# Optimization experiments

Hardware: AMD Instinct MI355X
Metric: run time of the kernel (lower is better)

Reference implementation:

```python
import jax, jax.numpy as jnp
import numpy as np

BN_EPS = 1e-5

def _bn(x, g, b, m, v):
    # eval-mode BatchNorm1d over channel dim of [B, C, N]
    scale = g / jnp.sqrt(v + BN_EPS)
    return (x - m[:, None]) * scale[:, None] + b[:, None]

def _conv1(W, x, b=None):
    # 1x1 Conv1d == channel matmul: W [O, C], x [B, C, N] -> [B, O, N]
    y = jnp.einsum('oc,bcn->bon', W, x)
    if b is not None:
        y = y + b[:, None]
    return y

def _sa_layer(x, wqk, wv, bv, wt, bt, g, b, m, v):
    # offset self-attention; q_conv and k_conv share weights
    xk = _conv1(wqk, x)                          # [B, D, N]
    xq = jnp.swapaxes(xk, 1, 2)                  # [B, N, D]
    xv = _conv1(wv, x, bv)                       # [B, D, N]
    energy = jnp.einsum('bnd,bdm->bnm', xq, xk)  # [B, N, N]
    attn = jax.nn.softmax(energy, axis=-1)
    attn = attn / (1e-9 + attn.sum(axis=1, keepdims=True))  # L1 renorm over dim=1
    x_r = jnp.einsum('bdn,bnm->bdm', xv, attn)   # [B, D, N]
    x_r = jax.nn.relu(_bn(_conv1(wt, x - x_r, bt), g, b, m, v))
    return x + x_r

def setup_inputs() -> dict:
    key = jax.random.key(0)
    ks = iter(jax.random.split(key, 64))
    B, Cin, N = 16, 3, 2048
    D, F, H1, OUT = 128, 1024, 512, 50
    def rn(shape, s=0.05):
        return jax.random.normal(next(ks), shape, dtype=jnp.float32) * s
    def var(shape):
        return jax.random.uniform(next(ks), shape, dtype=jnp.float32) * 0.5 + 0.5
    inp = {
        'x': jax.random.normal(next(ks), (B, Cin, N), dtype=jnp.float32),
        'w1': rn((D, Cin)), 'w2': rn((D, D)),
        'bn1_g': jnp.ones((D,)), 'bn1_b': jnp.zeros((D,)), 'bn1_m': rn((D,)), 'bn1_v': var((D,)),
        'bn2_g': jnp.ones((D,)), 'bn2_b': jnp.zeros((D,)), 'bn2_m': rn((D,)), 'bn2_v': var((D,)),
        'sa_wqk': rn((4, D, D)), 'sa_wv': rn((4, D, D)), 'sa_bv': rn((4, D)),
        'sa_wt': rn((4, D, D)), 'sa_bt': rn((4, D)),
        'sa_g': jnp.ones((4, D)), 'sa_b': jnp.zeros((4, D)), 'sa_m': rn((4, D)), 'sa_v': var((4, D)),
        'wf': rn((F, 4 * D)),
        'bnf_g': jnp.ones((F,)), 'bnf_b': jnp.zeros((F,)), 'bnf_m': rn((F,)), 'bnf_v': var((F,)),
        'ws1': rn((H1, 3 * F)), 'bs1': rn((H1,)),
        'bns1_g': jnp.ones((H1,)), 'bns1_b': jnp.zeros((H1,)), 'bns1_m': rn((H1,)), 'bns1_v': var((H1,)),
        'ws2': rn((OUT, H1)), 'bs2': rn((OUT,)),
        'bns2_g': jnp.ones((OUT,)), 'bns2_b': jnp.zeros((OUT,)), 'bns2_m': rn((OUT,)), 'bns2_v': var((OUT,)),
    }
    return inp

def reference(x, w1, w2, bn1_g, bn1_b, bn1_m, bn1_v, bn2_g, bn2_b, bn2_m, bn2_v,
              sa_wqk, sa_wv, sa_bv, sa_wt, sa_bt, sa_g, sa_b, sa_m, sa_v,
              wf, bnf_g, bnf_b, bnf_m, bnf_v,
              ws1, bs1, bns1_g, bns1_b, bns1_m, bns1_v,
              ws2, bs2, bns2_g, bns2_b, bns2_m, bns2_v):
    B, _, N = x.shape
    h = jax.nn.relu(_bn(_conv1(w1, x), bn1_g, bn1_b, bn1_m, bn1_v))
    h = jax.nn.relu(_bn(_conv1(w2, h), bn2_g, bn2_b, bn2_m, bn2_v))
    feats = []
    for i in range(4):
        h = _sa_layer(h, sa_wqk[i], sa_wv[i], sa_bv[i], sa_wt[i], sa_bt[i],
                      sa_g[i], sa_b[i], sa_m[i], sa_v[i])
        feats.append(h)
    cat = jnp.concatenate(feats, axis=1)                 # [B, 512, N]
    fused = _bn(_conv1(wf, cat), bnf_g, bnf_b, bnf_m, bnf_v)
    fused = jnp.where(fused >= 0, fused, 0.2 * fused)    # LeakyReLU(0.2)
    x_max = fused.max(axis=2)                            # [B, 1024]
    x_avg = fused.mean(axis=2)                           # [B, 1024]
    gmax = jnp.broadcast_to(x_max[:, :, None], (B, x_max.shape[1], N))
    gavg = jnp.broadcast_to(x_avg[:, :, None], (B, x_avg.shape[1], N))
    h = jnp.concatenate([fused, gmax, gavg], axis=1)     # [B, 3072, N]
    h = jax.nn.relu(_bn(_conv1(ws1, h, bs1), bns1_g, bns1_b, bns1_m, bns1_v))
    # dropout is identity in eval mode
    h = jax.nn.relu(_bn(_conv1(ws2, h, bs2), bns2_g, bns2_b, bns2_m, bns2_v))
    return h  # [B, out_channel, N]
```

## Files before the change

### kernel.cpp

```cpp
#include <hip/hip_runtime.h>
#include <cstdint>
#include <cstddef>

#define B_   16
#define N_   2048
#define D_   128
#define F_   1024
#define H1_  512
#define OUT_ 50

static constexpr float BN_EPS = 1e-5f;

typedef __attribute__((ext_vector_type(8))) short short8;
typedef __attribute__((ext_vector_type(4))) float f32x4;

__device__ inline unsigned short f2bf(float f) {
  union { float f; unsigned u; } v; v.f = f;
  unsigned r = v.u + 0x7fff + ((v.u >> 16) & 1);
  return (unsigned short)(r >> 16);
}
__device__ inline float bf2f(unsigned short h) {
  union { unsigned u; float f; } v; v.u = ((unsigned)h) << 16; return v.f;
}

__device__ inline void dma16(const unsigned short* g, unsigned short* l) {
  __builtin_amdgcn_global_load_lds(
      (const __attribute__((address_space(1))) unsigned int*)g,
      (__attribute__((address_space(3))) unsigned int*)l, 16, 0, 0);
}

__global__ void foldw_k(const float* __restrict__ W, int ldW,
                        const float* __restrict__ bias,
                        const float* __restrict__ g, const float* __restrict__ bb,
                        const float* __restrict__ m, const float* __restrict__ v,
                        unsigned short* __restrict__ Wb, float* __restrict__ biasF,
                        int O, int Opad, int K) {
  long i = (long)blockIdx.x * 256 + threadIdx.x;
  if (i >= (long)Opad * K) return;
  int o = (int)(i / K), k = (int)(i % K);
  float sc = 1.f, sh = 0.f;
  if (o < O && g) { sc = g[o] * rsqrtf(v[o] + BN_EPS); sh = bb[o] - m[o] * sc; }
  float w = (o < O) ? W[(long)o * ldW + k] * sc : 0.f;
  Wb[i] = f2bf(w);
  if (k == 0 && biasF) {
    float bf = 0.f;
    if (o < O) bf = (bias ? bias[o] : 0.f) * sc + sh;
    biasF[o] = bf;
  }
}

__global__ void conv1_k(const float* __restrict__ x, const float* __restrict__ w1,
                        const float* __restrict__ g, const float* __restrict__ bb,
                        const float* __restrict__ m, const float* __restrict__ v,
                        unsigned short* __restrict__ h0b) {
  int o = threadIdx.x, n = blockIdx.x, b = blockIdx.y;
  const float* xb = x + (long)b * 3 * N_;
  float val = w1[o * 3 + 0] * xb[n] + w1[o * 3 + 1] * xb[N_ + n] + w1[o * 3 + 2] * xb[2 * N_ + n];
  float sc = g[o] * rsqrtf(v[o] + BN_EPS);
  val = val * sc + (bb[o] - m[o] * sc);
  h0b[((long)b * N_ + n) * D_ + o] = f2bf(fmaxf(val, 0.f));
}

template <int TM>
__global__ __launch_bounds__(256, 4)
void gemm_tok(const unsigned short* __restrict__ Wb, int ldW,
              const unsigned short* __restrict__ A, long sA, int ldA,
              const float* __restrict__ biasF,
              const float* __restrict__ perBO, int ldPBO,
              const unsigned short* __restrict__ resH, long sRes, int ldRes,
              unsigned short* __restrict__ outH, long sOutH, int ldOutH,
              float* __restrict__ pmax, float* __restrict__ psum,
              int K, int act, int flags) {
  constexpr int MT = TM / 32;
  __shared__ unsigned short lAB[TM * 64 + 128 * 64];
  __shared__ float lpm[4][64], lps[4][64];
  unsigned short* lA = lAB;
  unsigned short* lB = lAB + TM * 64;
  unsigned short* lS = lAB;
  int tid = threadIdx.x;
  int n0 = blockIdx.x * TM, o0 = blockIdx.y * 128, b = blockIdx.z;
  int wave = tid >> 6, lane = tid & 63;
  int wr = wave >> 1, wc = wave & 1;
  int quad = lane >> 4, l15 = lane & 15;
  int rowL = lane >> 3;
  int kseg = (lane & 7) ^ rowL;
  const unsigned short* Ab = A + (long)b * sA + (long)n0 * ldA;
  const unsigned short* Wp = Wb + (long)o0 * ldW;

  f32x4 acc[MT][4];
  #pragma unroll
  for (int i = 0; i < MT; ++i)
    #pragma unroll
    for (int j = 0; j < 4; ++j) acc[i][j] = (f32x4){0.f, 0.f, 0.f, 0.f};

  for (int kc = 0; kc < K; kc += 64) {
    #pragma unroll
    for (int t = 0; t < 4; ++t) {
      int chunk = t * 4 + wave;
      dma16(Wp + (long)(chunk * 8 + rowL) * ldW + kc + kseg * 8, &lB[chunk * 512]);
      if (chunk < TM / 8)
        dma16(Ab + (long)(chunk * 8 + rowL) * ldA + kc + kseg * 8, &lA[chunk * 512]);
    }
    __syncthreads();
    #pragma unroll
    for (int kk = 0; kk < 2; ++kk) {
      short8 af[MT], bf[4];
      #pragma unroll
      for (int mt = 0; mt < MT; ++mt) {
        int r = wr * (TM / 2) + mt * 16 + l15;
        af[mt] = *(const short8*)&lA[r * 64 + (((kk * 4 + quad) ^ (l15 & 7)) * 8)];
      }
      #pragma unroll
      for (int ot = 0; ot < 4; ++ot) {
        int r = wc * 64 + ot * 16 + l15;
        bf[ot] = *(const short8*)&lB[r * 64 + (((kk * 4 + quad) ^ (l15 & 7)) * 8)];
      }
      #pragma unroll
      for (int mt = 0; mt < MT; ++mt)
        #pragma unroll
        for (int ot = 0; ot < 4; ++ot)
          acc[mt][ot] = __builtin_amdgcn_mfma_f32_16x16x32_bf16(bf[ot], af[mt], acc[mt][ot], 0, 0, 0);
    }
    __syncthreads();
  }

  bool doPool = (flags & 32) != 0;
  #pragma unroll
  for (int ot = 0; ot < 4; ++ot) {
    int obL = wc * 64 + ot * 16 + quad * 4;
    int ob = o0 + obL;
    float bi[4] = {0.f, 0.f, 0.f, 0.f};
    if (biasF) { float4 t = *(const float4*)&biasF[ob]; bi[0] = t.x; bi[1] = t.y; bi[2] = t.z; bi[3] = t.w; }
    if (perBO) {
      float4 t = *(const float4*)&perBO[(long)b * ldPBO + ob];
      bi[0] += t.x; bi[1] += t.y; bi[2] += t.z; bi[3] += t.w;
    }
    float pm4[4], ps4[4];
    #pragma unroll
    for (int r = 0; r < 4; ++r) { pm4[r] = -1e30f; ps4[r] = 0.f; }
    int g = obL >> 3, go = obL & 7;
    #pragma unroll
    for (int mt = 0; mt < MT; ++mt) {
      int nL = wr * (TM / 2) + mt * 16 + l15;
      float vals[4];
      #pragma unroll
      for (int r = 0; r < 4; ++r) {
        float val = acc[mt][ot][r] + bi[r];
        if (act == 1)      val = fmaxf(val, 0.f);
        else if (act == 2) val = (val >= 0.f) ? val : 0.2f * val;
        vals[r] = val;
      }
      if (flags & 16) {
        uint2 rv = *(const uint2*)&resH[(long)b * sRes + (long)(n0 + nL) * ldRes + ob];
        unsigned short rr[4];
        *(uint2*)rr = rv;
        #pragma unroll
        for (int r = 0; r < 4; ++r) vals[r] += bf2f(rr[r]);
      }
      unsigned short t4[4];
      #pragma unroll
      for (int r = 0; r < 4; ++r) {
        t4[r] = f2bf(vals[r]);
        if (doPool) { pm4[r] = fmaxf(pm4[r], vals[r]); ps4[r] += vals[r]; }
      }
      int gp = (g & 8) | ((g ^ (nL & 7)) & 7);
      *(uint2*)&lS[nL * 128 + gp * 8 + go] = *(uint2*)&t4[0];
    }
    if (doPool) {
      #pragma unroll
      for (int r = 0; r < 4; ++r) {
        float m = pm4[r], s = ps4[r];
        m = fmaxf(m, __shfl_xor(m, 1)); s += __shfl_xor(s, 1);
        m = fmaxf(m, __shfl_xor(m, 2)); s += __shfl_xor(s, 2);
        m = fmaxf(m, __shfl_xor(m, 4)); s += __shfl_xor(s, 4);
        m = fmaxf(m, __shfl_xor(m, 8)); s += __shfl_xor(s, 8);
        if (l15 == 0) { lpm[wave][ot * 16 + quad * 4 + r] = m; lps[wave][ot * 16 + quad * 4 + r] = s; }
      }
    }
  }
  __syncthreads();
  {
    int r0 = tid >> 4, s = tid & 15;
    #pragma unroll
    for (int it = 0; it < TM / 16; ++it) {
      int row = it * 16 + r0;
      int sp = (s & 8) | ((s ^ (row & 7)) & 7);
      short8 v = *(const short8*)&lS[row * 128 + sp * 8];
      *(short8*)&outH[(long)b * sOutH + (long)(n0 + row) * ldOutH + o0 + s * 8] = v;
    }
  }
  if (doPool && tid < 128) {
    int wcx = tid >> 6, ol = tid & 63;
    float m = fmaxf(lpm[wcx][ol], lpm[wcx + 2][ol]);
    float s = lps[wcx][ol] + lps[wcx + 2][ol];
    int o = o0 + wcx * 64 + ol;
    pmax[((long)b * 16 + blockIdx.x) * 1024 + o] = m;
    psum[((long)b * 16 + blockIdx.x) * 1024 + o] = s;
  }
}

template <int TM>
__global__ __launch_bounds__(256, 4)
void gemm_chan(const unsigned short* __restrict__ Wb, int ldW,
               const unsigned short* __restrict__ A, long sA, int ldA,
               const float* __restrict__ biasF,
               float* __restrict__ outF, long sOutF, int ldOutF,
               unsigned short* __restrict__ outH, long sOutH, int ldOutH,
               int K, int O, int act) {
  constexpr int MT = TM / 32;
  __shared__ unsigned short lA[TM * 64];
  __shared__ unsigned short lB[128 * 64];
  int tid = threadIdx.x;
  int n0 = blockIdx.x * TM, o0 = blockIdx.y * 128, b = blockIdx.z;
  int wave = tid >> 6, lane = tid & 63;
  int wr = wave >> 1, wc = wave & 1;
  int quad = lane >> 4, l15 = lane & 15;
  int rowL = lane >> 3;
  int kseg = (lane & 7) ^ rowL;
  const unsigned short* Ab = A + (long)b * sA + (long)n0 * ldA;
  const unsigned short* Wp = Wb + (long)o0 * ldW;

  f32x4 acc[MT][4];
  #pragma unroll
  for (int i = 0; i < MT; ++i)
    #pragma unroll
    for (int j = 0; j < 4; ++j) acc[i][j] = (f32x4){0.f, 0.f, 0.f, 0.f};

  for (int kc = 0; kc < K; kc += 64) {
    #pragma unroll
    for (int t = 0; t < 4; ++t) {
      int chunk = t * 4 + wave;
      dma16(Wp + (long)(chunk * 8 + rowL) * ldW + kc + kseg * 8, &lB[chunk * 512]);
      if (chunk < TM / 8)
        dma16(Ab + (long)(chunk * 8 + rowL) * ldA + kc + kseg * 8, &lA[chunk * 512]);
    }
    __syncthreads();
    #pragma unroll
    for (int kk = 0; kk < 2; ++kk) {
      short8 af[MT], bf[4];
      #pragma unroll
      for (int mt = 0; mt < MT; ++mt) {
        int r = wr * (TM / 2) + mt * 16 + l15;
        af[mt] = *(const short8*)&lA[r * 64 + (((kk * 4 + quad) ^ (l15 & 7)) * 8)];
      }
      #pragma unroll
      for (int ot = 0; ot < 4; ++ot) {
        int r = wc * 64 + ot * 16 + l15;
        bf[ot] = *(const short8*)&lB[r * 64 + (((kk * 4 + quad) ^ (l15 & 7)) * 8)];
      }
      #pragma unroll
      for (int mt = 0; mt < MT; ++mt)
        #pragma unroll
        for (int ot = 0; ot < 4; ++ot)
          acc[mt][ot] = __builtin_amdgcn_mfma_f32_16x16x32_bf16(af[mt], bf[ot], acc[mt][ot], 0, 0, 0);
    }
    __syncthreads();
  }

  #pragma unroll
  for (int ot = 0; ot < 4; ++ot) {
    int o = o0 + wc * 64 + ot * 16 + l15;
    if (o >= O) continue;
    float bi = biasF ? biasF[o] : 0.f;
    #pragma unroll
    for (int mt = 0; mt < MT; ++mt) {
      int nb = n0 + wr * (TM / 2) + mt * 16 + quad * 4;
      float vals[4];
      #pragma unroll
      for (int r = 0; r < 4; ++r) {
        float val = acc[mt][ot][r] + bi;
        if (act == 1)      val = fmaxf(val, 0.f);
        else if (act == 2) val = (val >= 0.f) ? val : 0.2f * val;
        vals[r] = val;
      }
      if (outF)
        *(float4*)&outF[(long)b * sOutF + (long)o * ldOutF + nb] = *(float4*)vals;
      if (outH) {
        unsigned short t[4];
        #pragma unroll
        for (int r = 0; r < 4; ++r) t[r] = f2bf(vals[r]);
        *(uint2*)&outH[(long)b * sOutH + (long)o * ldOutH + nb] = *(uint2*)&t[0];
      }
    }
  }
}

__global__ __launch_bounds__(256)
void gram_lw(const unsigned short* __restrict__ xk, long sXk,
             float* __restrict__ lw) {
  __shared__ unsigned short lK[2][64 * 128];
  int tid = threadIdx.x, wave = tid >> 6, lane = tid & 63;
  int quad = lane >> 4, l15 = lane & 15;
  int rowL4 = lane >> 4, s16 = lane & 15;
  int n0 = blockIdx.y * 64, b = blockIdx.x;
  const unsigned short* Kp = xk + (long)b * sXk;
  short8 afr[4];
  {
    const unsigned short* arow = Kp + (long)(n0 + wave * 16 + l15) * 128;
    #pragma unroll
    for (int kf = 0; kf < 4; ++kf) afr[kf] = *(const short8*)(arow + kf * 32 + quad * 8);
  }
  float runm[4], runs[4];
  #pragma unroll
  for (int r = 0; r < 4; ++r) { runm[r] = -1e30f; runs[r] = 0.f; }

  auto stage = [&](int ch, int bf) {
    #pragma unroll
    for (int t = 0; t < 4; ++t) {
      int c = t * 4 + wave;
      int row = c * 4 + rowL4;
      int gseg = (s16 & 8) | ((s16 ^ (row & 7)) & 7);
      dma16(Kp + (long)(ch * 64 + row) * 128 + gseg * 8, &lK[bf][c * 512]);
    }
  };
  stage(0, 0);

  for (int ch = 0; ch < 32; ++ch) {
    __syncthreads();
    int bf = ch & 1;
    if (ch + 1 < 32) stage(ch + 1, bf ^ 1);
    f32x4 sv[4];
    #pragma unroll
    for (int mf = 0; mf < 4; ++mf) {
      f32x4 s = (f32x4){0.f, 0.f, 0.f, 0.f};
      #pragma unroll
      for (int kf = 0; kf < 4; ++kf) {
        int r = mf * 16 + l15, q = kf * 4 + quad;
        int sp = (q & 8) | ((q ^ (r & 7)) & 7);
        short8 bfr = *(const short8*)&lK[bf][r * 128 + sp * 8];
        s = __builtin_amdgcn_mfma_f32_16x16x32_bf16(afr[kf], bfr, s, 0, 0, 0);
      }
      sv[mf] = s;
    }
    #pragma unroll
    for (int r = 0; r < 4; ++r) {
      float e0 = sv[0][r], e1 = sv[1][r], e2 = sv[2][r], e3 = sv[3][r];
      float cm = fmaxf(fmaxf(e0, e1), fmaxf(e2, e3));
      float mn = fmaxf(runm[r], cm);
      runs[r] = runs[r] * __expf(runm[r] - mn) +
                (__expf(e0 - mn) + __expf(e1 - mn)) + (__expf(e2 - mn) + __expf(e3 - mn));
      runm[r] = mn;
    }
  }
  #pragma unroll
  for (int r = 0; r < 4; ++r) {
    float m = runm[r], s = runs[r];
    #pragma unroll
    for (int off = 1; off < 16; off <<= 1) {
      float mo = __shfl_xor(m, off), so = __shfl_xor(s, off);
      float mn = fmaxf(m, mo);
      s = s * __expf(m - mn) + so * __expf(mo - mn);
      m = mn;
    }
    if (l15 == 0) {
      int n = n0 + wave * 16 + quad * 4 + r;
      lw[(long)b * 2048 + n] = m + __logf(s);
    }
  }
}

__global__ __launch_bounds__(256)
void pv_k(const unsigned short* __restrict__ xk, long sXk,
          const unsigned short* __restrict__ xv, long sXv,
          const float* __restrict__ lw,
          const unsigned short* __restrict__ lib, long sLi, int ldLi,
          unsigned short* __restrict__ xrb, long sXr) {
  __shared__ unsigned short lK[2][64 * 128];
  __shared__ unsigned short lV[2][128 * 64];
  __shared__ float lwt[2][64];
  int tid = threadIdx.x, wave = tid >> 6, lane = tid & 63;
  int quad = lane >> 4, l15 = lane & 15;
  int rowL4 = lane >> 4, s16 = lane & 15;
  int rowL8 = lane >> 3, s8 = lane & 7;
  int m0 = blockIdx.y * 64, b = blockIdx.x;
  const unsigned short* Kp = xk + (long)b * sXk;
  const unsigned short* Vp = xv + (long)b * sXv;
  short8 akr[4];
  {
    const unsigned short* arow = Kp + (long)(m0 + wave * 16 + l15) * 128;
    #pragma unroll
    for (int kf = 0; kf < 4; ++kf) akr[kf] = *(const short8*)(arow + kf * 32 + quad * 8);
  }
  f32x4 acc[8];
  #pragma unroll
  for (int dt = 0; dt < 8; ++dt) acc[dt] = (f32x4){0.f, 0.f, 0.f, 0.f};
  float runc = 0.f;

  auto stage = [&](int ch, int bf) {
    #pragma unroll
    for (int t = 0; t < 4; ++t) {
      int c = t * 4 + wave;
      int rowK = c * 4 + rowL4;
      int gsegK = (s16 & 8) | ((s16 ^ (rowK & 7)) & 7);
      dma16(Kp + (long)(ch * 64 + rowK) * 128 + gsegK * 8, &lK[bf][c * 512]);
      int rowV = c * 8 + rowL8;
      int gsegV = s8 ^ (rowV & 7);
      dma16(Vp + (long)rowV * 2048 + ch * 64 + gsegV * 8, &lV[bf][c * 512]);
    }
    if (tid < 64) lwt[bf][tid] = lw[(long)b * 2048 + ch * 64 + tid];
  };
  stage(0, 0);

  for (int ch = 0; ch < 32; ++ch) {
    __syncthreads();
    int bf = ch & 1;
    if (ch + 1 < 32) stage(ch + 1, bf ^ 1);
    unsigned pd0[4], pd1[4];
    #pragma unroll
    for (int nf = 0; nf < 4; ++nf) {
      f32x4 s = (f32x4){0.f, 0.f, 0.f, 0.f};
      #pragma unroll
      for (int kf = 0; kf < 4; ++kf) {
        int r = nf * 16 + l15, q = kf * 4 + quad;
        int sp = (q & 8) | ((q ^ (r & 7)) & 7);
        short8 kfr = *(const short8*)&lK[bf][r * 128 + sp * 8];
        s = __builtin_amdgcn_mfma_f32_16x16x32_bf16(kfr, akr[kf], s, 0, 0, 0);
      }
      float4 lw4 = *(const float4*)&lwt[bf][nf * 16 + quad * 4];
      float lwv[4] = {lw4.x, lw4.y, lw4.z, lw4.w};
      unsigned short t4[4];
      #pragma unroll
      for (int r = 0; r < 4; ++r) {
        float p = __expf(s[r] - lwv[r]);
        runc += p;
        t4[r] = f2bf(p);
      }
      pd0[nf] = (unsigned)t4[0] | ((unsigned)t4[1] << 16);
      pd1[nf] = (unsigned)t4[2] | ((unsigned)t4[3] << 16);
    }
    #pragma unroll
    for (int kc = 0; kc < 2; ++kc) {
      unsigned d0 = (quad >= 2) ? pd0[2 * kc + 1] : pd0[2 * kc];
      unsigned d1 = (quad >= 2) ? pd1[2 * kc + 1] : pd1[2 * kc];
      int s0 = ((quad & 1) << 5) + l15;
      union { unsigned u[4]; short8 v; } pu;
      pu.u[0] = (unsigned)__shfl((int)d0, s0);
      pu.u[1] = (unsigned)__shfl((int)d1, s0);
      pu.u[2] = (unsigned)__shfl((int)d0, s0 + 16);
      pu.u[3] = (unsigned)__shfl((int)d1, s0 + 16);
      short8 pa = pu.v;
      #pragma unroll
      for (int dt = 0; dt < 8; ++dt) {
        int r = dt * 16 + l15;
        int spv = (kc * 4 + quad) ^ (r & 7);
        short8 vb = *(const short8*)&lV[bf][r * 64 + spv * 8];
        acc[dt] = __builtin_amdgcn_mfma_f32_16x16x32_bf16(pa, vb, acc[dt], 0, 0, 0);
      }
    }
  }
  float s = runc;
  s += __shfl_xor(s, 16);
  s += __shfl_xor(s, 32);
  float inv = 1.f / (1e-9f + s);
  float inv4[4];
  #pragma unroll
  for (int r = 0; r < 4; ++r) inv4[r] = __shfl(inv, quad * 4 + r);
  #pragma unroll
  for (int dt = 0; dt < 8; ++dt) {
    int d = dt * 16 + l15;
    #pragma unroll
    for (int r = 0; r < 4; ++r) {
      int m = m0 + wave * 16 + quad * 4 + r;
      float lv = bf2f(lib[(long)b * sLi + (long)m * ldLi + d]);
      xrb[(long)b * sXr + (long)m * 128 + d] = f2bf(lv - acc[dt][r] * inv4[r]);
    }
  }
}

__global__ void poolred_k(const float* __restrict__ pmax, const float* __restrict__ psum,
                          float* __restrict__ xmax, float* __restrict__ xavg) {
  int f = blockIdx.x * 256 + threadIdx.x, b = blockIdx.y;
  float mx = -1e30f, s = 0.f;
  #pragma unroll
  for (int t = 0; t < 16; ++t) {
    mx = fmaxf(mx, pmax[((long)b * 16 + t) * 1024 + f]);
    s += psum[((long)b * 16 + t) * 1024 + f];
  }
  xmax[(long)b * 1024 + f] = mx;
  xavg[(long)b * 1024 + f] = s * (1.f / 2048.f);
}

__global__ __launch_bounds__(256)
void poolterm_k(const float* __restrict__ ws1, const float* __restrict__ xmax,
                const float* __restrict__ xavg,
                const float* __restrict__ bg, const float* __restrict__ bv,
                float* __restrict__ pt) {
  int o = blockIdx.x, b = blockIdx.y, tid = threadIdx.x;
  const float* w = ws1 + (long)o * 3072;
  float s = 0.f;
  #pragma unroll
  for (int it = 0; it < 4; ++it) {
    int c = tid + it * 256;
    s += w[1024 + c] * xmax[(long)b * 1024 + c] + w[2048 + c] * xavg[(long)b * 1024 + c];
  }
  #pragma unroll
  for (int off = 32; off; off >>= 1) s += __shfl_xor(s, off);
  __shared__ float rsm[4];
  if ((tid & 63) == 0) rsm[tid >> 6] = s;
  __syncthreads();
  if (tid == 0) {
    float sc = bg[o] * rsqrtf(bv[o] + BN_EPS);
    pt[(long)b * H1_ + o] = sc * (rsm[0] + rsm[1] + rsm[2] + rsm[3]);
  }
}

extern "C" void kernel_launch(void* const* d_in, const int* in_sizes, int n_in,
                              void* d_out, int out_size, void* d_ws, size_t ws_size,
                              hipStream_t stream) {
  const float* x      = (const float*)d_in[0];
  const float* w1     = (const float*)d_in[1];
  const float* w2     = (const float*)d_in[2];
  const float* bn1_g  = (const float*)d_in[3];
  const float* bn1_b  = (const float*)d_in[4];
  const float* bn1_m  = (const float*)d_in[5];
  const float* bn1_v  = (const float*)d_in[6];
  const float* bn2_g  = (const float*)d_in[7];
  const float* bn2_b  = (const float*)d_in[8];
  const float* bn2_m  = (const float*)d_in[9];
  const float* bn2_v  = (const float*)d_in[10];
  const float* sa_wqk = (const float*)d_in[11];
  const float* sa_wv  = (const float*)d_in[12];
  const float* sa_bv  = (const float*)d_in[13];
  const float* sa_wt  = (const float*)d_in[14];
  const float* sa_bt  = (const float*)d_in[15];
  const float* sa_g   = (const float*)d_in[16];
  const float* sa_b   = (const float*)d_in[17];
  const float* sa_m   = (const float*)d_in[18];
  const float* sa_v   = (const float*)d_in[19];
  const float* wf     = (const float*)d_in[20];
  const float* bnf_g  = (const float*)d_in[21];
  const float* bnf_b  = (const float*)d_in[22];
  const float* bnf_m  = (const float*)d_in[23];
  const float* bnf_v  = (const float*)d_in[24];
  const float* ws1    = (const float*)d_in[25];
  const float* bs1    = (const float*)d_in[26];
  const float* bns1_g = (const float*)d_in[27];
  const float* bns1_b = (const float*)d_in[28];
  const float* bns1_m = (const float*)d_in[29];
  const float* bns1_v = (const float*)d_in[30];
  const float* ws2    = (const float*)d_in[31];
  const float* bs2    = (const float*)d_in[32];
  const float* bns2_g = (const float*)d_in[33];
  const float* bns2_b = (const float*)d_in[34];
  const float* bns2_m = (const float*)d_in[35];
  const float* bns2_v = (const float*)d_in[36];
  float* out = (float*)d_out;

  float* ws = (float*)d_ws;
  size_t off = 0;
  auto alloc  = [&](size_t n) { float* p = ws + off; off += (n + 63) & ~(size_t)63; return p; };
  auto allocH = [&](size_t n) { return (unsigned short*)alloc((n + 1) / 2); };

  unsigned short* w2b  = allocH(128 * 128);
  unsigned short* wqkb = allocH(4 * 128 * 128);
  unsigned short* wvb  = allocH(4 * 128 * 128);
  unsigned short* wtb  = allocH(4 * 128 * 128);
  unsigned short* wfb  = allocH((size_t)F_ * 512);
  unsigned short* ws1b = allocH((size_t)H1_ * 1024);
  unsigned short* ws2b = allocH((size_t)128 * 512);
  float* bias_w2 = alloc(128);
  float* bias_v  = alloc(512);
  float* bias_t  = alloc(512);
  float* bias_f  = alloc(1024);
  float* bias_s1 = alloc(512);
  float* bias_s2 = alloc(128);
  float* lwB  = alloc((size_t)16 * 2048);
  float* pmax = alloc((size_t)16 * 16 * 1024);
  float* psum = alloc((size_t)16 * 16 * 1024);
  float* xmaxB = alloc((size_t)16 * 1024);
  float* xavgB = alloc((size_t)16 * 1024);
  float* ptB   = alloc((size_t)16 * 512);
  size_t fixedOff = off;

  const size_t perB = 131072 + 524288 + 1048576 + 131072 + 131072 + 131072;
  size_t wsFloats = ws_size / 4;
  int Gb = 1;
  for (int c : {16, 8, 4, 2, 1}) {
    if (fixedOff + (size_t)c * perB + 4096 <= wsFloats) { Gb = c; break; }
  }

  unsigned short* h1b    = allocH((size_t)Gb * 262144);
  unsigned short* featsb = allocH((size_t)Gb * 1048576);
  unsigned short* fusedb = allocH((size_t)Gb * 2097152);
  unsigned short* xkb    = allocH((size_t)Gb * 262144);
  unsigned short* xvb    = allocH((size_t)Gb * 262144);
  unsigned short* xrb    = allocH((size_t)Gb * 262144);
  unsigned short* h0b  = xrb;
  unsigned short* hs1b = featsb;

  foldw_k<<<64, 256, 0, stream>>>(w2, 128, nullptr, bn2_g, bn2_b, bn2_m, bn2_v,
                                  w2b, bias_w2, 128, 128, 128);
  for (int i = 0; i < 4; ++i) {
    foldw_k<<<64, 256, 0, stream>>>(sa_wqk + (size_t)i * 16384, 128, nullptr,
                                    nullptr, nullptr, nullptr, nullptr,
                                    wqkb + (size_t)i * 16384, nullptr, 128, 128, 128);
    foldw_k<<<64, 256, 0, stream>>>(sa_wv + (size_t)i * 16384, 128, sa_bv + i * 128,
                                    nullptr, nullptr, nullptr, nullptr,
                                    wvb + (size_t)i * 16384, bias_v + i * 128, 128, 128, 128);
    foldw_k<<<64, 256, 0, stream>>>(sa_wt + (size_t)i * 16384, 128, sa_bt + i * 128,
                                    sa_g + i * 128, sa_b + i * 128, sa_m + i * 128, sa_v + i * 128,
                                    wtb + (size_t)i * 16384, bias_t + i * 128, 128, 128, 128);
  }
  foldw_k<<<2048, 256, 0, stream>>>(wf, 512, nullptr, bnf_g, bnf_b, bnf_m, bnf_v,
                                    wfb, bias_f, 1024, 1024, 512);
  foldw_k<<<2048, 256, 0, stream>>>(ws1, 3072, bs1, bns1_g, bns1_b, bns1_m, bns1_v,
                                    ws1b, bias_s1, 512, 512, 1024);
  foldw_k<<<256, 256, 0, stream>>>(ws2, 512, bs2, bns2_g, bns2_b, bns2_m, bns2_v,
                                   ws2b, bias_s2, 50, 128, 512);

  const long sAct = 262144, sFeat = 1048576, sFus = 2097152;
  for (int b0 = 0; b0 < B_; b0 += Gb) {
    int g = Gb;
    conv1_k<<<dim3(N_, g), 128, 0, stream>>>(x + (long)b0 * 3 * N_, w1,
                                             bn1_g, bn1_b, bn1_m, bn1_v, h0b);
    gemm_tok<64><<<dim3(32, 1, g), 256, 0, stream>>>(
        w2b, 128, h0b, sAct, 128, bias_w2, nullptr, 0, nullptr, 0, 0,
        h1b, sAct, 128, nullptr, nullptr, 128, 1, 0);

    for (int i = 0; i < 4; ++i) {
      const unsigned short* lib = (i == 0) ? h1b : featsb + (size_t)(i - 1) * 128;
      int ldLi = (i == 0) ? 128 : 512;
      long sLi = (i == 0) ? sAct : sFeat;
      gemm_tok<64><<<dim3(32, 1, g), 256, 0, stream>>>(
          wqkb + (size_t)i * 16384, 128, lib, sLi, ldLi, nullptr, nullptr, 0,
          nullptr, 0, 0, xkb, sAct, 128, nullptr, nullptr, 128, 0, 0);
      gemm_chan<64><<<dim3(32, 1, g), 256, 0, stream>>>(
          wvb + (size_t)i * 16384, 128, lib, sLi, ldLi, bias_v + i * 128,
          nullptr, 0, 0, xvb, sAct, 2048, 128, 128, 0);
      gram_lw<<<dim3(g, 32), 256, 0, stream>>>(xkb, sAct, lwB);
      pv_k<<<dim3(g, 32), 256, 0, stream>>>(xkb, sAct, xvb, sAct, lwB,
                                            lib, sLi, ldLi, xrb, sAct);
      gemm_tok<64><<<dim3(32, 1, g), 256, 0, stream>>>(
          wtb + (size_t)i * 16384, 128, xrb, sAct, 128, bias_t + i * 128, nullptr, 0,
          lib, sLi, ldLi,
          featsb + (size_t)i * 128, sFeat, 512, nullptr, nullptr, 128, 1, 16);
    }

    gemm_tok<128><<<dim3(16, 8, g), 256, 0, stream>>>(
        wfb, 512, featsb, sFeat, 512, bias_f, nullptr, 0, nullptr, 0, 0,
        fusedb, sFus, 1024, pmax, psum, 512, 2, 32);
    poolred_k<<<dim3(4, g), 256, 0, stream>>>(pmax, psum, xmaxB, xavgB);
    poolterm_k<<<dim3(512, g), 256, 0, stream>>>(ws1, xmaxB, xavgB, bns1_g, bns1_v, ptB);
    gemm_tok<128><<<dim3(16, 4, g), 256, 0, stream>>>(
        ws1b, 1024, fusedb, sFus, 1024, bias_s1, ptB, 512, nullptr, 0, 0,
        hs1b, sFeat, 512, nullptr, nullptr, 1024, 1, 0);
    gemm_chan<64><<<dim3(32, 1, g), 256, 0, stream>>>(
        ws2b, 512, hs1b, sFeat, 512, bias_s2,
        out + (long)b0 * OUT_ * N_, (long)OUT_ * N_, 2048, nullptr, 0, 0,
        512, 50, 1);
  }
}
```

Measured before the change: 787.9 us.

## Split attention reductions over two key segments with separate combine kernels

The row-softmax statistics kernel and the P·V kernel now split the 2048-long reduction into two halves along a third grid dimension. This doubles the number of blocks and shortens each block's serial loop. Partial max/sum values and partial fp32 accumulators are written out, then combined by two new small reduction kernels. The P·V kernel also drops LDS double-buffering in favour of a single buffer with two barriers per chunk, which lowers LDS use per block. The cost is extra global traffic for the fp32 partials (about 2 MB per batch), two more launches per layer, and lost overlap of loads with compute.

```diff
diff --git a/kernel.cpp b/kernel.cpp
--- a/kernel.cpp
+++ b/kernel.cpp
@@ -287,12 +287,13 @@
 
 __global__ __launch_bounds__(256)
 void gram_lw(const unsigned short* __restrict__ xk, long sXk,
-             float* __restrict__ lw) {
+             float* __restrict__ pm, float* __restrict__ ps) {
   __shared__ unsigned short lK[2][64 * 128];
   int tid = threadIdx.x, wave = tid >> 6, lane = tid & 63;
   int quad = lane >> 4, l15 = lane & 15;
   int rowL4 = lane >> 4, s16 = lane & 15;
-  int n0 = blockIdx.y * 64, b = blockIdx.x;
+  int n0 = blockIdx.y * 64, b = blockIdx.x, seg = blockIdx.z;
+  int mbase = seg * 1024;
   const unsigned short* Kp = xk + (long)b * sXk;
   short8 afr[4];
   {
@@ -310,15 +311,15 @@
       int c = t * 4 + wave;
       int row = c * 4 + rowL4;
       int gseg = (s16 & 8) | ((s16 ^ (row & 7)) & 7);
-      dma16(Kp + (long)(ch * 64 + row) * 128 + gseg * 8, &lK[bf][c * 512]);
+      dma16(Kp + (long)(mbase + ch * 64 + row) * 128 + gseg * 8, &lK[bf][c * 512]);
     }
   };
   stage(0, 0);
 
-  for (int ch = 0; ch < 32; ++ch) {
+  for (int ch = 0; ch < 16; ++ch) {
     __syncthreads();
     int bf = ch & 1;
-    if (ch + 1 < 32) stage(ch + 1, bf ^ 1);
+    if (ch + 1 < 16) stage(ch + 1, bf ^ 1);
     f32x4 sv[4];
     #pragma unroll
     for (int mf = 0; mf < 4; ++mf) {
@@ -354,25 +355,36 @@
     }
     if (l15 == 0) {
       int n = n0 + wave * 16 + quad * 4 + r;
-      lw[(long)b * 2048 + n] = m + __logf(s);
-    }
-  }
+      pm[((long)b * 2 + seg) * 2048 + n] = m;
+      ps[((long)b * 2 + seg) * 2048 + n] = s;
+    }
+  }
+}
+
+__global__ void lwred_k(const float* __restrict__ pm, const float* __restrict__ ps,
+                        float* __restrict__ lw) {
+  int n = blockIdx.x * 256 + threadIdx.x, b = blockIdx.y;
+  float m0 = pm[((long)b * 2) * 2048 + n], m1 = pm[((long)b * 2 + 1) * 2048 + n];
+  float s0 = ps[((long)b * 2) * 2048 + n], s1 = ps[((long)b * 2 + 1) * 2048 + n];
+  float mx = fmaxf(m0, m1);
+  float s = s0 * __expf(m0 - mx) + s1 * __expf(m1 - mx);
+  lw[(long)b * 2048 + n] = mx + __logf(s);
 }
 
 __global__ __launch_bounds__(256)
 void pv_k(const unsigned short* __restrict__ xk, long sXk,
           const unsigned short* __restrict__ xv, long sXv,
           const float* __restrict__ lw,
-          const unsigned short* __restrict__ lib, long sLi, int ldLi,
-          unsigned short* __restrict__ xrb, long sXr) {
-  __shared__ unsigned short lK[2][64 * 128];
-  __shared__ unsigned short lV[2][128 * 64];
-  __shared__ float lwt[2][64];
+          float* __restrict__ pacc, float* __restrict__ pc) {
+  __shared__ unsigned short lK[64 * 128];
+  __shared__ unsigned short lV[128 * 64];
+  __shared__ float lwt[64];
   int tid = threadIdx.x, wave = tid >> 6, lane = tid & 63;
   int quad = lane >> 4, l15 = lane & 15;
   int rowL4 = lane >> 4, s16 = lane & 15;
   int rowL8 = lane >> 3, s8 = lane & 7;
-  int m0 = blockIdx.y * 64, b = blockIdx.x;
+  int m0 = blockIdx.y * 64, b = blockIdx.x, seg = blockIdx.z;
+  int nbase = seg * 1024;
   const unsigned short* Kp = xk + (long)b * sXk;
   const unsigned short* Vp = xv + (long)b * sXv;
   short8 akr[4];
@@ -386,25 +398,20 @@
   for (int dt = 0; dt < 8; ++dt) acc[dt] = (f32x4){0.f, 0.f, 0.f, 0.f};
   float runc = 0.f;
 
-  auto stage = [&](int ch, int bf) {
+  for (int ch = 0; ch < 16; ++ch) {
+    if (ch) __syncthreads();
     #pragma unroll
     for (int t = 0; t < 4; ++t) {
       int c = t * 4 + wave;
       int rowK = c * 4 + rowL4;
       int gsegK = (s16 & 8) | ((s16 ^ (rowK & 7)) & 7);
-      dma16(Kp + (long)(ch * 64 + rowK) * 128 + gsegK * 8, &lK[bf][c * 512]);
+      dma16(Kp + (long)(nbase + ch * 64 + rowK) * 128 + gsegK * 8, &lK[c * 512]);
       int rowV = c * 8 + rowL8;
       int gsegV = s8 ^ (rowV & 7);
-      dma16(Vp + (long)rowV * 2048 + ch * 64 + gsegV * 8, &lV[bf][c * 512]);
-    }
-    if (tid < 64) lwt[bf][tid] = lw[(long)b * 2048 + ch * 64 + tid];
-  };
-  stage(0, 0);
-
-  for (int ch = 0; ch < 32; ++ch) {
+      dma16(Vp + (long)rowV * 2048 + nbase + ch * 64 + gsegV * 8, &lV[c * 512]);
+    }
+    if (tid < 64) lwt[tid] = lw[(long)b * 2048 + nbase + ch * 64 + tid];
     __syncthreads();
-    int bf = ch & 1;
-    if (ch + 1 < 32) stage(ch + 1, bf ^ 1);
     unsigned pd0[4], pd1[4];
     #pragma unroll
     for (int nf = 0; nf < 4; ++nf) {
@@ -413,10 +420,10 @@
       for (int kf = 0; kf < 4; ++kf) {
         int r = nf * 16 + l15, q = kf * 4 + quad;
         int sp = (q & 8) | ((q ^ (r & 7)) & 7);
-        short8 kfr = *(const short8*)&lK[bf][r * 128 + sp * 8];
+        short8 kfr = *(const short8*)&lK[r * 128 + sp * 8];
         s = __builtin_amdgcn_mfma_f32_16x16x32_bf16(kfr, akr[kf], s, 0, 0, 0);
       }
-      float4 lw4 = *(const float4*)&lwt[bf][nf * 16 + quad * 4];
+      float4 lw4 = *(const float4*)&lwt[nf * 16 + quad * 4];
       float lwv[4] = {lw4.x, lw4.y, lw4.z, lw4.w};
       unsigned short t4[4];
       #pragma unroll
@@ -443,7 +450,7 @@
       for (int dt = 0; dt < 8; ++dt) {
         int r = dt * 16 + l15;
         int spv = (kc * 4 + quad) ^ (r & 7);
-        short8 vb = *(const short8*)&lV[bf][r * 64 + spv * 8];
+        short8 vb = *(const short8*)&lV[r * 64 + spv * 8];
         acc[dt] = __builtin_amdgcn_mfma_f32_16x16x32_bf16(pa, vb, acc[dt], 0, 0, 0);
       }
     }
@@ -451,20 +458,38 @@
   float s = runc;
   s += __shfl_xor(s, 16);
   s += __shfl_xor(s, 32);
-  float inv = 1.f / (1e-9f + s);
-  float inv4[4];
-  #pragma unroll
-  for (int r = 0; r < 4; ++r) inv4[r] = __shfl(inv, quad * 4 + r);
+  if (quad == 0)
+    pc[((long)b * 2 + seg) * 2048 + m0 + wave * 16 + l15] = s;
+  float* pa = pacc + ((long)b * 2 + seg) * 262144;
   #pragma unroll
   for (int dt = 0; dt < 8; ++dt) {
     int d = dt * 16 + l15;
     #pragma unroll
-    for (int r = 0; r < 4; ++r) {
-      int m = m0 + wave * 16 + quad * 4 + r;
-      float lv = bf2f(lib[(long)b * sLi + (long)m * ldLi + d]);
-      xrb[(long)b * sXr + (long)m * 128 + d] = f2bf(lv - acc[dt][r] * inv4[r]);
-    }
-  }
+    for (int r = 0; r < 4; ++r)
+      pa[(long)(m0 + wave * 16 + quad * 4 + r) * 128 + d] = acc[dt][r];
+  }
+}
+
+__global__ __launch_bounds__(256)
+void pvred_k(const float* __restrict__ pacc, const float* __restrict__ pc,
+             const unsigned short* __restrict__ lib, long sLi, int ldLi,
+             unsigned short* __restrict__ xrb, long sXr) {
+  int i = blockIdx.x * 256 + threadIdx.x;
+  int b = blockIdx.y;
+  int m = i >> 5, d4 = (i & 31) * 4;
+  float4 a0 = *(const float4*)&pacc[((long)b * 2 + 0) * 262144 + (long)m * 128 + d4];
+  float4 a1 = *(const float4*)&pacc[((long)b * 2 + 1) * 262144 + (long)m * 128 + d4];
+  float c = pc[((long)b * 2) * 2048 + m] + pc[((long)b * 2 + 1) * 2048 + m];
+  float inv = 1.f / (1e-9f + c);
+  uint2 lv = *(const uint2*)&lib[(long)b * sLi + (long)m * ldLi + d4];
+  unsigned short lr[4];
+  *(uint2*)lr = lv;
+  unsigned short o[4];
+  o[0] = f2bf(bf2f(lr[0]) - (a0.x + a1.x) * inv);
+  o[1] = f2bf(bf2f(lr[1]) - (a0.y + a1.y) * inv);
+  o[2] = f2bf(bf2f(lr[2]) - (a0.z + a1.z) * inv);
+  o[3] = f2bf(bf2f(lr[3]) - (a0.w + a1.w) * inv);
+  *(uint2*)&xrb[(long)b * sXr + (long)m * 128 + d4] = *(uint2*)&o[0];
 }
 
 __global__ void poolred_k(const float* __restrict__ pmax, const float* __restrict__ psum,
@@ -572,7 +597,8 @@
   float* ptB   = alloc((size_t)16 * 512);
   size_t fixedOff = off;
 
-  const size_t perB = 131072 + 524288 + 1048576 + 131072 + 131072 + 131072;
+  const size_t perB = 131072 + 524288 + 1048576 + 131072 + 131072 + 131072 +
+                      524288 + 12288;
   size_t wsFloats = ws_size / 4;
   int Gb = 1;
   for (int c : {16, 8, 4, 2, 1}) {
@@ -585,6 +611,10 @@
   unsigned short* xkb    = allocH((size_t)Gb * 262144);
   unsigned short* xvb    = allocH((size_t)Gb * 262144);
   unsigned short* xrb    = allocH((size_t)Gb * 262144);
+  float* paccB = alloc((size_t)Gb * 2 * 262144);
+  float* pmB   = alloc((size_t)Gb * 2 * 2048);
+  float* psB   = alloc((size_t)Gb * 2 * 2048);
+  float* pcB   = alloc((size_t)Gb * 2 * 2048);
   unsigned short* h0b  = xrb;
   unsigned short* hs1b = featsb;
 
@@ -627,9 +657,10 @@
       gemm_chan<64><<<dim3(32, 1, g), 256, 0, stream>>>(
           wvb + (size_t)i * 16384, 128, lib, sLi, ldLi, bias_v + i * 128,
           nullptr, 0, 0, xvb, sAct, 2048, 128, 128, 0);
-      gram_lw<<<dim3(g, 32), 256, 0, stream>>>(xkb, sAct, lwB);
-      pv_k<<<dim3(g, 32), 256, 0, stream>>>(xkb, sAct, xvb, sAct, lwB,
-                                            lib, sLi, ldLi, xrb, sAct);
+      gram_lw<<<dim3(g, 32, 2), 256, 0, stream>>>(xkb, sAct, pmB, psB);
+      lwred_k<<<dim3(8, g), 256, 0, stream>>>(pmB, psB, lwB);
+      pv_k<<<dim3(g, 32, 2), 256, 0, stream>>>(xkb, sAct, xvb, sAct, lwB, paccB, pcB);
+      pvred_k<<<dim3(256, g), 256, 0, stream>>>(paccB, pcB, lib, sLi, ldLi, xrb, sAct);
       gemm_tok<64><<<dim3(32, 1, g), 256, 0, stream>>>(
           wtb + (size_t)i * 16384, 128, xrb, sAct, 128, bias_t + i * 128, nullptr, 0,
           lib, sLi, ldLi,
```

After: 786.0 us. No clear change (-0.2%).
